# Kernel tuning notes

Hardware: AMD Instinct MI355X
Metric: run time of the kernel (lower is better)

## Reference

```python
import jax, jax.numpy as jnp
import numpy as np

NUM_HEADS = 8

def _proj(x, W, b):
    # 1x1 conv == per-pixel linear: x [b,c,h,w], W [c_out,c_in], b [c_out]
    return jnp.einsum('bchw,oc->bohw', x, W) + b[None, :, None, None]

def setup_inputs() -> dict:
    key = jax.random.key(0)
    ks = jax.random.split(key, 5)
    b, c, h, w = 2, 256, 64, 64
    s = 0.02
    return {
        'x1': jax.random.normal(ks[0], (b, c, h, w), jnp.float32),
        'Wq': jax.random.normal(ks[1], (c, c), jnp.float32) * s,
        'bq': jnp.zeros((c,), jnp.float32),
        'Wk': jax.random.normal(ks[2], (c, c), jnp.float32) * s,
        'bk': jnp.zeros((c,), jnp.float32),
        'Wv': jax.random.normal(ks[3], (c, c), jnp.float32) * s,
        'bv': jnp.zeros((c,), jnp.float32),
        'Wo': jax.random.normal(ks[4], (c, c), jnp.float32) * s,
        'bo': jnp.zeros((c,), jnp.float32),
    }

def reference(x1, Wq, bq, Wk, bk, Wv, bv, Wo, bo):
    b, c, h, w = x1.shape
    H = NUM_HEADS
    d = c // H
    n = h * w
    scale = d ** -0.5

    def to_heads(t):
        # [b,c,h,w] -> 'b c h w -> b (h w) c' -> 'b n (H d) -> b H n d'
        # channel order: head index is the outer factor of c
        return t.reshape(b, H, d, n).transpose(0, 1, 3, 2)  # [b,H,n,d]

    q = to_heads(_proj(x1, Wq, bq))
    k = to_heads(_proj(x1, Wk, bk))
    v = to_heads(_proj(x1, Wv, bv))

    attn = jnp.einsum('bhnd,bhmd->bhnm', q, k) * scale  # [b,H,n,n]
    attn = jax.nn.softmax(attn, axis=-1)
    out = jnp.einsum('bhnm,bhmd->bhnd', attn, v)        # [b,H,n,d]
    # 'b H n d -> b n (H d)' -> 'b (h w) c -> b c h w'
    out = out.transpose(0, 2, 1, 3).reshape(b, n, c).transpose(0, 2, 1).reshape(b, c, h, w)
    return _proj(out, Wo, bo)
```

## Files before the change

### kernel.cpp

```cpp
#include <hip/hip_runtime.h>
#include <cmath>


typedef unsigned int u32;
typedef unsigned short u16;
typedef __attribute__((ext_vector_type(4))) float f32x4;
typedef __attribute__((ext_vector_type(16))) float f32x16;
typedef __attribute__((ext_vector_type(8))) short short8;
typedef __attribute__((ext_vector_type(4))) u32 u32x4;

__device__ __forceinline__ u32 cvtpk_bf16(float a, float b) {
  u32 r; asm("v_cvt_pk_bf16_f32 %0, %1, %2" : "=v"(r) : "v"(a), "v"(b)); return r;
}
__device__ __forceinline__ u16 f2bf(float x) { return (u16)cvtpk_bf16(x, x); }

__device__ __forceinline__ f32x16 mfma16(short8 a, short8 b, f32x16 c) {
  return __builtin_amdgcn_mfma_f32_32x32x16_bf16(a, b, c, 0, 0, 0);
}

__device__ __forceinline__ void split2(float a, float b, u32 &hw, u32 &lw) {
  u32 ua = __builtin_bit_cast(u32, a), ub = __builtin_bit_cast(u32, b);
  hw = (ua >> 16) | (ub & 0xffff0000u);
  float ra = a - __builtin_bit_cast(float, ua & 0xffff0000u);
  float rb = b - __builtin_bit_cast(float, ub & 0xffff0000u);
  lw = cvtpk_bf16(ra, rb);
}
__device__ __forceinline__ void split8(f32x4 a, f32x4 b, short8 &hf, short8 &lf) {
  u32 h0,l0,h1,l1,h2,l2,h3,l3;
  split2(a[0],a[1],h0,l0); split2(a[2],a[3],h1,l1);
  split2(b[0],b[1],h2,l2); split2(b[2],b[3],h3,l3);
  u32x4 hv = {h0,h1,h2,h3}, lv = {l0,l1,l2,l3};
  hf = __builtin_bit_cast(short8, hv);
  lf = __builtin_bit_cast(short8, lv);
}

__device__ __forceinline__ int rowmap(int r, int hi) {
  return (r & 3) + 8 * ((r >> 2) & 1) + 4 * hi + 16 * (r >> 3);
}
__device__ __forceinline__ int tau(int kv) {
  return (kv & 19) | ((kv & 4) << 1) | ((kv & 8) >> 1);
}

#define QMUL (0.17677669529663689f * 1.4426950408889634f)
#define WPLANE 65536
#define WMAT  131072

__global__ __launch_bounds__(256) void prep_kernel(
    const float* __restrict__ X,
    const float* __restrict__ Wq, const float* __restrict__ Wk,
    const float* __restrict__ Wv, const float* __restrict__ Wo,
    u16* __restrict__ Xa, u16* __restrict__ Wpk)
{
  const int bx = blockIdx.x, tid = threadIdx.x;
  if (bx < 256) {
    __shared__ float lt[32 * 257];
    const int b = bx >> 7, ntile = bx & 127, n0 = ntile * 32;
    const int nn = tid & 31, cg = tid >> 5;
    #pragma unroll 4
    for (int i = 0; i < 32; i++) {
      int c = i * 8 + cg;
      lt[nn * 257 + c] = X[((size_t)b * 256 + c) * 4096 + n0 + nn];
    }
    __syncthreads();
    const int lane = tid & 63, w = tid >> 6;
    const int l31 = lane & 31, fh = lane >> 5;
    #pragma unroll
    for (int kk = 0; kk < 4; kk++) {
      int kt = w * 4 + kk;
      const float* p = &lt[l31 * 257 + kt * 16 + fh * 8];
      u32x4 pk = { cvtpk_bf16(p[0],p[1]), cvtpk_bf16(p[2],p[3]),
                   cvtpk_bf16(p[4],p[5]), cvtpk_bf16(p[6],p[7]) };
      *(u32x4*)(&Xa[(((size_t)b * 128 + ntile) * 16 + kt) * 512 + lane * 8]) = pk;
    }
  } else {
    const int j = (bx - 256) * 256 + tid;
    const int lane = j & 63, ct = (j >> 6) & 7, kt = (j >> 9) & 15, mat = j >> 13;
    const float* W = mat == 0 ? Wq : (mat == 1 ? Wk : (mat == 2 ? Wv : Wo));
    const int c = ct * 32 + (lane & 31);
    const int k0 = kt * 16 + (lane >> 5) * 8;
    f32x4 a = *(const f32x4*)(W + (size_t)c * 256 + k0);
    f32x4 b = *(const f32x4*)(W + (size_t)c * 256 + k0 + 4);
    if (mat == 0) {
      #pragma unroll
      for (int i = 0; i < 4; i++) { a[i] *= QMUL; b[i] *= QMUL; }
    }
    short8 wh, wl; split8(a, b, wh, wl);
    size_t base = ((size_t)mat * 2) * WPLANE + ((size_t)kt * 8 + ct) * 512 + lane * 8;
    *(short8*)(&Wpk[base]) = wh;
    *(short8*)(&Wpk[base + WPLANE]) = wl;
  }
}

__global__ __launch_bounds__(256) void qkv_kernel(
    const u16* __restrict__ Xa, const u16* __restrict__ Wpk,
    const float* __restrict__ bq, const float* __restrict__ bk,
    const float* __restrict__ bv,
    u16* __restrict__ Qf, u16* __restrict__ Kf, u16* __restrict__ V3)
{
  const int z = blockIdx.z, mode = z % 3, b = z / 3;
  const int tid = threadIdx.x, lane = tid & 63, wv = tid >> 6;
  const int ntile = blockIdx.x;
  const int l31 = lane & 31, fh = lane >> 5;

  const u16* Amat = Xa + ((size_t)b * 128 + ntile) * 8192;
  const u16* Bmat = Wpk + (size_t)mode * WMAT;

  f32x16 acc[2] = {{}, {}};
  for (int kt = 0; kt < 16; kt++) {
    short8 xa = *(const short8*)(Amat + kt * 512 + lane * 8);
    #pragma unroll
    for (int i = 0; i < 2; i++) {
      int ct = wv * 2 + i;
      const u16* wp = Bmat + ((size_t)kt * 8 + ct) * 512 + lane * 8;
      short8 wh = *(const short8*)(wp);
      short8 wl = *(const short8*)(wp + WPLANE);
      acc[i] = mfma16(wh, xa, acc[i]);
      acc[i] = mfma16(wl, xa, acc[i]);
    }
  }

  const float* bias = mode == 0 ? bq : (mode == 1 ? bk : bv);
  const float bscale = mode == 0 ? QMUL : 1.0f;

  if (mode == 2) {
    const int sl = tau(l31);
    #pragma unroll
    for (int i = 0; i < 2; i++) {
      int head = wv * 2 + i;
      size_t tb = ((size_t)(b * 8 + head) * 128 + ntile) * 1024;
      #pragma unroll
      for (int r = 0; r < 16; r++) {
        int dv = rowmap(r, fh);
        V3[tb + (size_t)dv * 32 + sl] = f2bf(acc[i][r] + bias[head * 32 + dv]);
      }
    }
  } else {
    u16* Out = mode == 0 ? Qf : Kf;
    #pragma unroll
    for (int i = 0; i < 2; i++) {
      int head = wv * 2 + i;
      size_t nb = ((size_t)(b * 8 + head) * 128 + ntile) * 1024;
      #pragma unroll
      for (int kt2 = 0; kt2 < 2; kt2++) {
        float v[8];
        #pragma unroll
        for (int e = 0; e < 8; e++) {
          int c = head * 32 + rowmap(kt2 * 8 + e, fh);
          v[e] = acc[i][kt2 * 8 + e] + bscale * bias[c];
        }
        u32x4 pk = { cvtpk_bf16(v[0],v[1]), cvtpk_bf16(v[2],v[3]),
                     cvtpk_bf16(v[4],v[5]), cvtpk_bf16(v[6],v[7]) };
        *(u32x4*)(&Out[nb + (size_t)kt2 * 512 + lane * 8]) = pk;
      }
    }
  }
}

__global__ __launch_bounds__(256, 3) void attn_kernel(
    const u16* __restrict__ Qf, const u16* __restrict__ Kf,
    const u16* __restrict__ V3, u16* __restrict__ OaH, u16* __restrict__ OaL)
{
  const int fid = blockIdx.x;
  const int xcd = fid & 7, j = fid >> 3;
  const int bh = xcd + 8 * (j >> 6);
  const int qgrp = j & 63;
  const int b = bh >> 3, h = bh & 7;

  const int tid = threadIdx.x, wv = tid >> 6, lane = tid & 63;
  const int l31 = lane & 31, fh = lane >> 5;

  const u16* qfb = Qf + (size_t)bh * 131072 + (size_t)(qgrp * 2) * 1024 + lane * 8;
  short8 qa0 = *(const short8*)(qfb);
  short8 qa1 = *(const short8*)(qfb + 512);
  short8 qb0 = *(const short8*)(qfb + 1024);
  short8 qb1 = *(const short8*)(qfb + 1536);

  const u16* kfb = Kf + (size_t)bh * 131072;
  const u16* vfb = V3 + (size_t)bh * 131072;

  const u32x4 onesu = {0x3F803F80u, 0x3F803F80u, 0x3F803F80u, 0x3F803F80u};
  const short8 ones = __builtin_bit_cast(short8, onesu);

  f32x16 accA = {}, accB = {}, sumA = {}, sumB = {};

  for (int it = 0; it < 32; it++) {
    const int kvt = wv * 32 + it;
    const u16* kp = kfb + (size_t)kvt * 1024 + lane * 8;
    const u16* vp = vfb + (size_t)kvt * 1024 + l31 * 32 + fh * 8;
    short8 kc0 = *(const short8*)(kp);
    short8 kc1 = *(const short8*)(kp + 512);
    short8 vc0 = *(const short8*)(vp);
    short8 vc1 = *(const short8*)(vp + 16);

    f32x16 sA = {}, sB = {};
    sA = mfma16(kc0, qa0, sA);
    sA = mfma16(kc1, qa1, sA);
    sB = mfma16(kc0, qb0, sB);
    sB = mfma16(kc1, qb1, sB);

    #pragma unroll
    for (int r = 0; r < 16; r++) sA[r] = __builtin_amdgcn_exp2f(sA[r]);
    u32x4 uA0 = { cvtpk_bf16(sA[0],sA[1]),  cvtpk_bf16(sA[2],sA[3]),
                  cvtpk_bf16(sA[4],sA[5]),  cvtpk_bf16(sA[6],sA[7]) };
    u32x4 uA1 = { cvtpk_bf16(sA[8],sA[9]),  cvtpk_bf16(sA[10],sA[11]),
                  cvtpk_bf16(sA[12],sA[13]),cvtpk_bf16(sA[14],sA[15]) };
    short8 pA0 = __builtin_bit_cast(short8, uA0);
    short8 pA1 = __builtin_bit_cast(short8, uA1);
    accA = mfma16(vc0, pA0, accA);
    accA = mfma16(vc1, pA1, accA);
    sumA = mfma16(ones, pA0, sumA);
    sumA = mfma16(ones, pA1, sumA);

    #pragma unroll
    for (int r = 0; r < 16; r++) sB[r] = __builtin_amdgcn_exp2f(sB[r]);
    u32x4 uB0 = { cvtpk_bf16(sB[0],sB[1]),  cvtpk_bf16(sB[2],sB[3]),
                  cvtpk_bf16(sB[4],sB[5]),  cvtpk_bf16(sB[6],sB[7]) };
    u32x4 uB1 = { cvtpk_bf16(sB[8],sB[9]),  cvtpk_bf16(sB[10],sB[11]),
                  cvtpk_bf16(sB[12],sB[13]),cvtpk_bf16(sB[14],sB[15]) };
    short8 pB0 = __builtin_bit_cast(short8, uB0);
    short8 pB1 = __builtin_bit_cast(short8, uB1);
    accB = mfma16(vc0, pB0, accB);
    accB = mfma16(vc1, pB1, accB);
    sumB = mfma16(ones, pB0, sumB);
    sumB = mfma16(ones, pB1, sumB);
  }

  __shared__ float accb[2][4][64][17];
  __shared__ float lsb[2][4][64];

  #pragma unroll
  for (int r = 0; r < 16; r++) { accb[0][wv][lane][r] = accA[r]; accb[1][wv][lane][r] = accB[r]; }
  lsb[0][wv][lane] = sumA[0];
  lsb[1][wv][lane] = sumB[0];
  __syncthreads();

  const int set = wv & 1, ktl = wv >> 1;
  const float Lt = (lsb[set][0][l31] + lsb[set][1][l31]) +
                   (lsb[set][2][l31] + lsb[set][3][l31]);
  const float Linv = 1.0f / Lt;

  float o[8];
  #pragma unroll
  for (int e = 0; e < 8; e++) {
    int hs = (e >> 2) & 1;
    int r = (e & 3) + 4 * fh + 8 * ktl;
    int li = hs * 32 + l31;
    o[e] = Linv * ((accb[set][0][li][r] + accb[set][1][li][r]) +
                   (accb[set][2][li][r] + accb[set][3][li][r]));
  }
  f32x4 o0 = {o[0], o[1], o[2], o[3]}, o1 = {o[4], o[5], o[6], o[7]};
  short8 oh, ol; split8(o0, o1, oh, ol);
  const int qt = qgrp * 2 + set, ktg = h * 2 + ktl;
  size_t addr = (((size_t)b * 128 + qt) * 16 + ktg) * 512 + lane * 8;
  *(short8*)(&OaH[addr]) = oh;
  *(short8*)(&OaL[addr]) = ol;
}

__global__ __launch_bounds__(256) void oproj_kernel(
    const u16* __restrict__ OaH, const u16* __restrict__ OaL,
    const u16* __restrict__ Wpk, const float* __restrict__ bo,
    float* __restrict__ Out)
{
  const int b = blockIdx.z, ct = blockIdx.y;
  const int tid = threadIdx.x, lane = tid & 63, wv = tid >> 6;
  const int ntile = blockIdx.x * 4 + wv;
  const int l31 = lane & 31, fh = lane >> 5;

  const u16* Wo = Wpk + (size_t)3 * WMAT;
  const u16* Ob = OaH + ((size_t)b * 128 + ntile) * 8192;
  const u16* Ol = OaL + ((size_t)b * 128 + ntile) * 8192;

  f32x16 acc = {};
  for (int kt = 0; kt < 16; kt++) {
    const u16* wp = Wo + ((size_t)kt * 8 + ct) * 512 + lane * 8;
    short8 wh = *(const short8*)(wp);
    short8 wl = *(const short8*)(wp + WPLANE);
    short8 oh = *(const short8*)(Ob + kt * 512 + lane * 8);
    short8 ol = *(const short8*)(Ol + kt * 512 + lane * 8);
    acc = mfma16(wh, oh, acc);
    acc = mfma16(wh, ol, acc);
    acc = mfma16(wl, oh, acc);
  }
  #pragma unroll
  for (int r = 0; r < 16; r++) {
    int c = ct * 32 + rowmap(r, fh);
    Out[((size_t)b * 256 + c) * 4096 + ntile * 32 + l31] = acc[r] + bo[c];
  }
}

extern "C" void kernel_launch(void* const* d_in, const int* in_sizes, int n_in,
                              void* d_out, int out_size, void* d_ws, size_t ws_size,
                              hipStream_t stream) {
  const float* x1 = (const float*)d_in[0];
  const float* Wq = (const float*)d_in[1];
  const float* bq = (const float*)d_in[2];
  const float* Wk = (const float*)d_in[3];
  const float* bk = (const float*)d_in[4];
  const float* Wv = (const float*)d_in[5];
  const float* bv = (const float*)d_in[6];
  const float* Wo = (const float*)d_in[7];
  const float* bo = (const float*)d_in[8];

  const size_t NEL = (size_t)2 * 4096 * 256;
  u16* Xa  = (u16*)d_ws;
  u16* Qf  = Xa + NEL;
  u16* Kf  = Qf + NEL;
  u16* V3  = Kf + NEL;
  u16* OaL = V3 + NEL;
  u16* Wpk = OaL + NEL;
  u16* OaH = Xa;
  float* out = (float*)d_out;

  prep_kernel<<<dim3(384), 256, 0, stream>>>(x1, Wq, Wk, Wv, Wo, Xa, Wpk);
  qkv_kernel<<<dim3(128, 1, 6), 256, 0, stream>>>(Xa, Wpk, bq, bk, bv, Qf, Kf, V3);
  attn_kernel<<<dim3(1024), 256, 0, stream>>>(Qf, Kf, V3, OaH, OaL);
  oproj_kernel<<<dim3(32, 8, 2), 256, 0, stream>>>(OaH, OaL, Wpk, bo, out);
}
```

Before: 140.8 us.

## Split attention KV loop across 8 waves and compute row sums with VALU adds

The attention kernel now launches 512 threads per block, so each of 8 waves handles 16 KV tiles instead of 32, doubling wave-level parallelism per query group. The softmax denominators are now accumulated with scalar float adds plus a cross-half shuffle instead of extra MFMA ops against a ones matrix, removing a quarter of the MFMA work in the loop. The trade-off is a larger shared-memory reduction buffer (8 partials), an 8-way reduction at the end where only 4 waves write output, and different occupancy pressure from the new launch bounds.

```diff
diff --git a/kernel.cpp b/kernel.cpp
--- a/kernel.cpp
+++ b/kernel.cpp
@@ -156,7 +156,7 @@
   }
 }
 
-__global__ __launch_bounds__(256, 3) void attn_kernel(
+__global__ __launch_bounds__(512, 4) void attn_kernel(
     const u16* __restrict__ Qf, const u16* __restrict__ Kf,
     const u16* __restrict__ V3, u16* __restrict__ OaH, u16* __restrict__ OaL)
 {
@@ -178,13 +178,11 @@
   const u16* kfb = Kf + (size_t)bh * 131072;
   const u16* vfb = V3 + (size_t)bh * 131072;
 
-  const u32x4 onesu = {0x3F803F80u, 0x3F803F80u, 0x3F803F80u, 0x3F803F80u};
-  const short8 ones = __builtin_bit_cast(short8, onesu);
-
-  f32x16 accA = {}, accB = {}, sumA = {}, sumB = {};
-
-  for (int it = 0; it < 32; it++) {
-    const int kvt = wv * 32 + it;
+  f32x16 accA = {}, accB = {};
+  float lsA0 = 0.f, lsA1 = 0.f, lsB0 = 0.f, lsB1 = 0.f;
+
+  for (int it = 0; it < 16; it++) {
+    const int kvt = wv * 16 + it;
     const u16* kp = kfb + (size_t)kvt * 1024 + lane * 8;
     const u16* vp = vfb + (size_t)kvt * 1024 + l31 * 32 + fh * 8;
     short8 kc0 = *(const short8*)(kp);
@@ -192,68 +190,72 @@
     short8 vc0 = *(const short8*)(vp);
     short8 vc1 = *(const short8*)(vp + 16);
 
-    f32x16 sA = {}, sB = {};
-    sA = mfma16(kc0, qa0, sA);
-    sA = mfma16(kc1, qa1, sA);
-    sB = mfma16(kc0, qb0, sB);
-    sB = mfma16(kc1, qb1, sB);
-
-    #pragma unroll
-    for (int r = 0; r < 16; r++) sA[r] = __builtin_amdgcn_exp2f(sA[r]);
-    u32x4 uA0 = { cvtpk_bf16(sA[0],sA[1]),  cvtpk_bf16(sA[2],sA[3]),
-                  cvtpk_bf16(sA[4],sA[5]),  cvtpk_bf16(sA[6],sA[7]) };
-    u32x4 uA1 = { cvtpk_bf16(sA[8],sA[9]),  cvtpk_bf16(sA[10],sA[11]),
-                  cvtpk_bf16(sA[12],sA[13]),cvtpk_bf16(sA[14],sA[15]) };
-    short8 pA0 = __builtin_bit_cast(short8, uA0);
-    short8 pA1 = __builtin_bit_cast(short8, uA1);
-    accA = mfma16(vc0, pA0, accA);
-    accA = mfma16(vc1, pA1, accA);
-    sumA = mfma16(ones, pA0, sumA);
-    sumA = mfma16(ones, pA1, sumA);
-
-    #pragma unroll
-    for (int r = 0; r < 16; r++) sB[r] = __builtin_amdgcn_exp2f(sB[r]);
-    u32x4 uB0 = { cvtpk_bf16(sB[0],sB[1]),  cvtpk_bf16(sB[2],sB[3]),
-                  cvtpk_bf16(sB[4],sB[5]),  cvtpk_bf16(sB[6],sB[7]) };
-    u32x4 uB1 = { cvtpk_bf16(sB[8],sB[9]),  cvtpk_bf16(sB[10],sB[11]),
-                  cvtpk_bf16(sB[12],sB[13]),cvtpk_bf16(sB[14],sB[15]) };
-    short8 pB0 = __builtin_bit_cast(short8, uB0);
-    short8 pB1 = __builtin_bit_cast(short8, uB1);
-    accB = mfma16(vc0, pB0, accB);
-    accB = mfma16(vc1, pB1, accB);
-    sumB = mfma16(ones, pB0, sumB);
-    sumB = mfma16(ones, pB1, sumB);
-  }
-
-  __shared__ float accb[2][4][64][17];
-  __shared__ float lsb[2][4][64];
-
+    {
+      f32x16 s = {};
+      s = mfma16(kc0, qa0, s);
+      s = mfma16(kc1, qa1, s);
+      #pragma unroll
+      for (int r = 0; r < 16; r++) s[r] = __builtin_amdgcn_exp2f(s[r]);
+      lsA0 += ((s[0]+s[1]) + (s[2]+s[3])) + ((s[4]+s[5]) + (s[6]+s[7]));
+      lsA1 += ((s[8]+s[9]) + (s[10]+s[11])) + ((s[12]+s[13]) + (s[14]+s[15]));
+      u32x4 u0 = { cvtpk_bf16(s[0],s[1]),  cvtpk_bf16(s[2],s[3]),
+                   cvtpk_bf16(s[4],s[5]),  cvtpk_bf16(s[6],s[7]) };
+      u32x4 u1 = { cvtpk_bf16(s[8],s[9]),  cvtpk_bf16(s[10],s[11]),
+                   cvtpk_bf16(s[12],s[13]),cvtpk_bf16(s[14],s[15]) };
+      accA = mfma16(vc0, __builtin_bit_cast(short8,u0), accA);
+      accA = mfma16(vc1, __builtin_bit_cast(short8,u1), accA);
+    }
+    {
+      f32x16 s = {};
+      s = mfma16(kc0, qb0, s);
+      s = mfma16(kc1, qb1, s);
+      #pragma unroll
+      for (int r = 0; r < 16; r++) s[r] = __builtin_amdgcn_exp2f(s[r]);
+      lsB0 += ((s[0]+s[1]) + (s[2]+s[3])) + ((s[4]+s[5]) + (s[6]+s[7]));
+      lsB1 += ((s[8]+s[9]) + (s[10]+s[11])) + ((s[12]+s[13]) + (s[14]+s[15]));
+      u32x4 u0 = { cvtpk_bf16(s[0],s[1]),  cvtpk_bf16(s[2],s[3]),
+                   cvtpk_bf16(s[4],s[5]),  cvtpk_bf16(s[6],s[7]) };
+      u32x4 u1 = { cvtpk_bf16(s[8],s[9]),  cvtpk_bf16(s[10],s[11]),
+                   cvtpk_bf16(s[12],s[13]),cvtpk_bf16(s[14],s[15]) };
+      accB = mfma16(vc0, __builtin_bit_cast(short8,u0), accB);
+      accB = mfma16(vc1, __builtin_bit_cast(short8,u1), accB);
+    }
+  }
+
+  __shared__ float accb[2][8][64][17];
+  __shared__ float lsb[2][8][64];
+
+  { float ls = lsA0 + lsA1; ls += __shfl_xor(ls, 32); lsb[0][wv][lane] = ls; }
+  { float ls = lsB0 + lsB1; ls += __shfl_xor(ls, 32); lsb[1][wv][lane] = ls; }
   #pragma unroll
   for (int r = 0; r < 16; r++) { accb[0][wv][lane][r] = accA[r]; accb[1][wv][lane][r] = accB[r]; }
-  lsb[0][wv][lane] = sumA[0];
-  lsb[1][wv][lane] = sumB[0];
   __syncthreads();
 
-  const int set = wv & 1, ktl = wv >> 1;
-  const float Lt = (lsb[set][0][l31] + lsb[set][1][l31]) +
-                   (lsb[set][2][l31] + lsb[set][3][l31]);
-  const float Linv = 1.0f / Lt;
-
-  float o[8];
-  #pragma unroll
-  for (int e = 0; e < 8; e++) {
-    int hs = (e >> 2) & 1;
-    int r = (e & 3) + 4 * fh + 8 * ktl;
-    int li = hs * 32 + l31;
-    o[e] = Linv * ((accb[set][0][li][r] + accb[set][1][li][r]) +
-                   (accb[set][2][li][r] + accb[set][3][li][r]));
-  }
-  f32x4 o0 = {o[0], o[1], o[2], o[3]}, o1 = {o[4], o[5], o[6], o[7]};
-  short8 oh, ol; split8(o0, o1, oh, ol);
-  const int qt = qgrp * 2 + set, ktg = h * 2 + ktl;
-  size_t addr = (((size_t)b * 128 + qt) * 16 + ktg) * 512 + lane * 8;
-  *(short8*)(&OaH[addr]) = oh;
-  *(short8*)(&OaL[addr]) = ol;
+  if (wv < 4) {
+    const int set = wv >> 1, ktl = wv & 1;
+    float Lt = 0.f;
+    #pragma unroll
+    for (int w2 = 0; w2 < 8; w2++) Lt += lsb[set][w2][l31];
+    const float Linv = 1.0f / Lt;
+
+    float o[8];
+    #pragma unroll
+    for (int e = 0; e < 8; e++) {
+      int hs = (e >> 2) & 1;
+      int r = (e & 3) + 4 * fh + 8 * ktl;
+      int li = hs * 32 + l31;
+      float v = 0.f;
+      #pragma unroll
+      for (int w2 = 0; w2 < 8; w2++) v += accb[set][w2][li][r];
+      o[e] = v * Linv;
+    }
+    f32x4 o0 = {o[0], o[1], o[2], o[3]}, o1 = {o[4], o[5], o[6], o[7]};
+    short8 oh, ol; split8(o0, o1, oh, ol);
+    const int qt = qgrp * 2 + set, ktg = h * 2 + ktl;
+    size_t addr = (((size_t)b * 128 + qt) * 16 + ktg) * 512 + lane * 8;
+    *(short8*)(&OaH[addr]) = oh;
+    *(short8*)(&OaL[addr]) = ol;
+  }
 }
 
 __global__ __launch_bounds__(256) void oproj_kernel(
@@ -313,6 +315,6 @@
 
   prep_kernel<<<dim3(384), 256, 0, stream>>>(x1, Wq, Wk, Wv, Wo, Xa, Wpk);
   qkv_kernel<<<dim3(128, 1, 6), 256, 0, stream>>>(Xa, Wpk, bq, bk, bv, Qf, Kf, V3);
-  attn_kernel<<<dim3(1024), 256, 0, stream>>>(Qf, Kf, V3, OaH, OaL);
+  attn_kernel<<<dim3(1024), 512, 0, stream>>>(Qf, Kf, V3, OaH, OaL);
   oproj_kernel<<<dim3(32, 8, 2), 256, 0, stream>>>(OaH, OaL, Wpk, bo, out);
 }
```

After: 141.2 us. About the same (+0.3%).
